# Kernel tuning notes

Measured on AMD Instinct MI355X. Metric: run time of the kernel, lower is better.

## Reference

```python
import jax, jax.numpy as jnp
import numpy as np

H = 1024        # hidden_size
NH = 16         # num_attention_heads
DH = H // NH    # head dim = 64
I = 4096        # intermediate_size
E = 8           # moe_num_experts
B, S = 2, 2048
EPS = 1e-12


def _ln(x, g, b):
    mu = jnp.mean(x, axis=-1, keepdims=True)
    var = jnp.mean(jnp.square(x - mu), axis=-1, keepdims=True)
    return (x - mu) * jax.lax.rsqrt(var + EPS) * g + b


def setup_inputs() -> dict:
    key = jax.random.key(0)
    ks = jax.random.split(key, 16)
    std = 0.02
    p = {
        "hidden_states": jax.random.normal(ks[0], (B, S, H), jnp.float32),
        "Wq": jax.random.normal(ks[1], (H, H), jnp.float32) * std,
        "bq": jnp.zeros((H,), jnp.float32),
        "Wk": jax.random.normal(ks[2], (H, H), jnp.float32) * std,
        "bk": jnp.zeros((H,), jnp.float32),
        "Wv": jax.random.normal(ks[3], (H, H), jnp.float32) * std,
        "bv": jnp.zeros((H,), jnp.float32),
        "Wao": jax.random.normal(ks[4], (H, H), jnp.float32) * std,
        "bao": jnp.zeros((H,), jnp.float32),
        "ln1_g": jnp.ones((H,), jnp.float32),
        "ln1_b": jnp.zeros((H,), jnp.float32),
        "router_w": jax.random.normal(ks[5], (H, E), jnp.float32) * std,
        "We": jax.random.normal(ks[6], (E, H, I), jnp.float32) * std,
        "be": jnp.zeros((E, I), jnp.float32),
        "Wo": jax.random.normal(ks[7], (I, H), jnp.float32) * std,
        "bo": jnp.zeros((H,), jnp.float32),
        "ln2_g": jnp.ones((H,), jnp.float32),
        "ln2_b": jnp.zeros((H,), jnp.float32),
    }
    return p


def reference(hidden_states, Wq, bq, Wk, bk, Wv, bv, Wao, bao, ln1_g, ln1_b,
              router_w, We, be, Wo, bo, ln2_g, ln2_b):
    x = hidden_states  # [B,S,H]

    def heads(t):  # [B,S,H] -> [B,NH,S,DH]
        return t.reshape(B, S, NH, DH).transpose(0, 2, 1, 3)

    q = heads(x @ Wq + bq)
    k = heads(x @ Wk + bk)
    v = heads(x @ Wv + bv)
    scores = jnp.einsum("bhqd,bhkd->bhqk", q, k) / jnp.sqrt(jnp.float32(DH))
    probs = jax.nn.softmax(scores, axis=-1)
    ctx = jnp.einsum("bhqk,bhkd->bhqd", probs, v)
    ctx = ctx.transpose(0, 2, 1, 3).reshape(B, S, H)
    attn_out = _ln(ctx @ Wao + bao + x, ln1_g, ln1_b)  # BertSelfOutput

    # ---- MoE FFN: top-1 routing, per-expert GELU MLP, shared output proj ----
    flat = attn_out.reshape(-1, H)              # [N,H]
    logits = flat @ router_w                    # [N,E]
    idx = jnp.argmax(logits, axis=-1)           # top-1 of softmax == argmax of logits
    inter = jnp.zeros((flat.shape[0], I), flat.dtype)
    for e in range(E):  # small fixed expert count
        h_e = jax.nn.gelu(flat @ We[e] + be[e], approximate=False)
        inter = jnp.where((idx == e)[:, None], h_e, inter)
    inter = inter.reshape(B, S, I)
    out = _ln(inter @ Wo + bo + attn_out, ln2_g, ln2_b)  # BertOutput
    return out
```

## Files before the change

kernel.cpp:

```cpp
#include <hip/hip_runtime.h>
#include <hip/hip_bf16.h>
#include <cstdint>

#define H_  1024
#define NH_ 16
#define DH_ 64
#define I_  4096
#define E_  8
#define B_  2
#define S_  2048
#define N_  4096
#define QKVLD 3072
#define LN_EPS 1e-12f

typedef __attribute__((ext_vector_type(4))) float f4;
typedef __attribute__((ext_vector_type(8))) short s8v;
typedef unsigned int u32;

__device__ __forceinline__ float bf2f(unsigned short u) {
  union { unsigned int i; float f; } c; c.i = ((unsigned int)u) << 16; return c.f;
}
__device__ __forceinline__ unsigned short f2bf(float f) {
  __hip_bfloat16 h = __float2bfloat16(f);
  return *reinterpret_cast<unsigned short*>(&h);
}
__device__ __forceinline__ u32 pack_bf2(float a, float b) {
  return (u32)f2bf(a) | ((u32)f2bf(b) << 16);
}
__device__ __forceinline__ float gelu_f(float x) {
  return 0.5f * x * (1.0f + erff(x * 0.70710678118f));
}
__device__ __forceinline__ void gload16(const void* g, void* l) {
  __builtin_amdgcn_global_load_lds(
      (const __attribute__((address_space(1))) void*)g,
      (__attribute__((address_space(3))) void*)l, 16, 0, 0);
}

__global__ __launch_bounds__(256) void cvt_bf16_kernel(
    const float* __restrict__ in, ushort* __restrict__ out, int n8)
{
  const int t = blockIdx.x * 256 + threadIdx.x;
  if (t >= n8) return;
  const f4 x0 = *(const f4*)(in + (size_t)t * 8);
  const f4 x1 = *(const f4*)(in + (size_t)t * 8 + 4);
  s8v o;
#pragma unroll
  for (int j = 0; j < 4; ++j) { o[j] = (short)f2bf(x0[j]); o[4 + j] = (short)f2bf(x1[j]); }
  *(s8v*)(out + (size_t)t * 8) = o;
}

__global__ __launch_bounds__(256) void transpose_cvt_kernel(
    const float* __restrict__ in, ushort* __restrict__ out, int R, int C)
{
  __shared__ float tile[32][33];
  const size_t zo = (size_t)blockIdx.z * R * C;
  const int bx = blockIdx.x << 5, by = blockIdx.y << 5;
  const int tx = threadIdx.x & 31, ty = threadIdx.x >> 5;
  const float* ip = in + zo + (size_t)by * C + bx;
#pragma unroll
  for (int i = 0; i < 4; ++i)
    tile[ty + 8 * i][tx] = ip[(size_t)(ty + 8 * i) * C + tx];
  __syncthreads();
  ushort* op = out + zo + (size_t)bx * R + by;
#pragma unroll
  for (int i = 0; i < 4; ++i)
    op[(size_t)(ty + 8 * i) * R + tx] = f2bf(tile[tx][ty + 8 * i]);
}

__global__ void concat3_kernel(const float* a, const float* b, const float* c,
                               float* __restrict__ o)
{
  const int t = blockIdx.x * 256 + threadIdx.x;
  if (t < 1024) o[t] = a[t];
  else if (t < 2048) o[t] = b[t - 1024];
  else o[t] = c[t - 2048];
}

__global__ __launch_bounds__(256) void gather_kernel(
    const ushort* __restrict__ X, const int* __restrict__ lists,
    ushort* __restrict__ Xg)
{
  const int r = (blockIdx.x << 1) + (threadIdx.x >> 7);
  const int c = (threadIdx.x & 127) << 3;
  const int tok = lists[r];
  *(s8v*)&Xg[(size_t)r * H_ + c] = *(const s8v*)&X[(size_t)tok * H_ + c];
}

template <bool BF16OUT, int KSPLIT>
__global__ __launch_bounds__(256, 3) void gemm_mfma_kernel(
    const ushort* __restrict__ A, const ushort* __restrict__ Bt,
    const float* __restrict__ bias, void* __restrict__ Cout,
    const int M, const int N, const int K)
{
  __shared__ __align__(16) ushort Asm[2][4][128][8];
  __shared__ __align__(16) ushort Bsm[2][4][128][8];
  const int tid = threadIdx.x;
  const int w = tid >> 6, l = tid & 63;
  const int lq = l & 15, g = l >> 4;
  const int wm = w >> 1, wn = w & 1;
  const int nbx = N >> 7;
  const int nwg = nbx * (M >> 7);
  int id = blockIdx.y * nbx + blockIdx.x;
  id = (id & 7) * (nwg >> 3) + (id >> 3);
  const int m0 = (id / nbx) << 7, n0 = (id % nbx) << 7;
  const int Kspan = K / KSPLIT;
  const int kbase = (KSPLIT > 1) ? blockIdx.z * Kspan : 0;

  const ushort* a0 = A + (size_t)(m0 + l) * K + kbase + (w << 3);
  const ushort* a1 = a0 + (size_t)64 * K;
  const ushort* b0 = Bt + (size_t)(n0 + l) * K + kbase + (w << 3);
  const ushort* b1 = b0 + (size_t)64 * K;

  f4 acc[4][4] = {};
  const int nt = Kspan >> 5;
  gload16(a0, &Asm[0][w][0][0]);  gload16(a1, &Asm[0][w][64][0]);
  gload16(b0, &Bsm[0][w][0][0]);  gload16(b1, &Bsm[0][w][64][0]);
  __syncthreads();
  int cur = 0;
  for (int t = 0; t < nt; ++t) {
    if (t + 1 < nt) {
      const int kt = (t + 1) << 5;
      gload16(a0 + kt, &Asm[cur ^ 1][w][0][0]);
      gload16(a1 + kt, &Asm[cur ^ 1][w][64][0]);
      gload16(b0 + kt, &Bsm[cur ^ 1][w][0][0]);
      gload16(b1 + kt, &Bsm[cur ^ 1][w][64][0]);
    }
    s8v af[4], bfv[4];
#pragma unroll
    for (int mi = 0; mi < 4; ++mi)
      af[mi] = *(const s8v*)&Asm[cur][g][(wm << 6) + (mi << 4) + lq][0];
#pragma unroll
    for (int ni = 0; ni < 4; ++ni)
      bfv[ni] = *(const s8v*)&Bsm[cur][g][(wn << 6) + (ni << 4) + lq][0];
#pragma unroll
    for (int mi = 0; mi < 4; ++mi)
#pragma unroll
      for (int ni = 0; ni < 4; ++ni)
        acc[mi][ni] = __builtin_amdgcn_mfma_f32_16x16x32_bf16(af[mi], bfv[ni], acc[mi][ni], 0, 0, 0);
    __syncthreads();
    cur ^= 1;
  }
  if constexpr (BF16OUT) {
    ushort* st = (ushort*)Asm + (size_t)w * (16 * 72);
    float bs[4];
#pragma unroll
    for (int ni = 0; ni < 4; ++ni) bs[ni] = bias[n0 + (wn << 6) + (ni << 4) + lq];
#pragma unroll
    for (int mi = 0; mi < 4; ++mi) {
#pragma unroll
      for (int ni = 0; ni < 4; ++ni)
#pragma unroll
        for (int r = 0; r < 4; ++r)
          st[((g << 2) + r) * 72 + (ni << 4) + lq] = f2bf(acc[mi][ni][r] + bs[ni]);
#pragma unroll
      for (int q2 = 0; q2 < 2; ++q2) {
        const int r16 = l & 15, ch = (l >> 4) + (q2 << 2);
        const s8v vv = *(const s8v*)&st[r16 * 72 + (ch << 3)];
        *(s8v*)&((ushort*)Cout)[(size_t)(m0 + (wm << 6) + (mi << 4) + r16) * N
                                + n0 + (wn << 6) + (ch << 3)] = vv;
      }
    }
  } else {
    float* outf = (float*)Cout + (size_t)blockIdx.z * M * N;
#pragma unroll
    for (int ni = 0; ni < 4; ++ni) {
      const int col = n0 + (wn << 6) + (ni << 4) + lq;
      const float bs = (KSPLIT == 1 || blockIdx.z == 0) ? bias[col] : 0.f;
#pragma unroll
      for (int mi = 0; mi < 4; ++mi) {
        const int row = m0 + (wm << 6) + (mi << 4) + (g << 2);
#pragma unroll
        for (int r = 0; r < 4; ++r)
          outf[(size_t)(row + r) * N + col] = acc[mi][ni][r] + bs;
      }
    }
  }
}

__global__ __launch_bounds__(256, 3) void moe_mfma_kernel(
    const ushort* __restrict__ Xg, const ushort* __restrict__ WeT,
    const float* __restrict__ be, const int* __restrict__ lists,
    const int* __restrict__ offs, const int* __restrict__ cnt,
    const int* __restrict__ tb, ushort* __restrict__ inter)
{
  __shared__ __align__(16) ushort Asm[2][4][128][8];
  __shared__ __align__(16) ushort Bsm[2][4][128][8];
  __shared__ int tokL[128];
  const int by = blockIdx.y;
  if (by >= tb[E_]) return;
  int e = 0;
#pragma unroll
  for (int t = 1; t < E_; ++t) if (by >= tb[t]) e = t;
  const int rt = by - tb[e];
  const int base = offs[e] + (rt << 7);
  const int nrows = cnt[e] - (rt << 7);
  const int tid = threadIdx.x;
  if (tid < 128) tokL[tid] = (tid < nrows) ? lists[base + tid] : -1;
  __syncthreads();
  const int w = tid >> 6, l = tid & 63;
  const int lq = l & 15, g = l >> 4;
  const int wm = w >> 1, wn = w & 1;
  const int n0 = blockIdx.x << 7;
  const int r0 = min(base + l, N_ - 1);
  const int r1 = min(base + 64 + l, N_ - 1);
  const ushort* a0 = Xg + (size_t)r0 * H_ + (w << 3);
  const ushort* a1 = Xg + (size_t)r1 * H_ + (w << 3);
  const ushort* Wp = WeT + (size_t)e * I_ * H_;
  const ushort* b0 = Wp + (size_t)(n0 + l) * H_ + (w << 3);
  const ushort* b1 = b0 + (size_t)64 * H_;

  f4 acc[4][4] = {};
  gload16(a0, &Asm[0][w][0][0]);  gload16(a1, &Asm[0][w][64][0]);
  gload16(b0, &Bsm[0][w][0][0]);  gload16(b1, &Bsm[0][w][64][0]);
  __syncthreads();
  int cur = 0;
  for (int t = 0; t < 32; ++t) {
    if (t + 1 < 32) {
      const int kt = (t + 1) << 5;
      gload16(a0 + kt, &Asm[cur ^ 1][w][0][0]);
      gload16(a1 + kt, &Asm[cur ^ 1][w][64][0]);
      gload16(b0 + kt, &Bsm[cur ^ 1][w][0][0]);
      gload16(b1 + kt, &Bsm[cur ^ 1][w][64][0]);
    }
    s8v af[4], bfv[4];
#pragma unroll
    for (int mi = 0; mi < 4; ++mi)
      af[mi] = *(const s8v*)&Asm[cur][g][(wm << 6) + (mi << 4) + lq][0];
#pragma unroll
    for (int ni = 0; ni < 4; ++ni)
      bfv[ni] = *(const s8v*)&Bsm[cur][g][(wn << 6) + (ni << 4) + lq][0];
#pragma unroll
    for (int mi = 0; mi < 4; ++mi)
#pragma unroll
      for (int ni = 0; ni < 4; ++ni)
        acc[mi][ni] = __builtin_amdgcn_mfma_f32_16x16x32_bf16(af[mi], bfv[ni], acc[mi][ni], 0, 0, 0);
    __syncthreads();
    cur ^= 1;
  }
  {
    ushort* st = (ushort*)Asm + (size_t)w * (16 * 72);
    float bs[4];
#pragma unroll
    for (int ni = 0; ni < 4; ++ni) bs[ni] = be[(size_t)e * I_ + n0 + (wn << 6) + (ni << 4) + lq];
#pragma unroll
    for (int mi = 0; mi < 4; ++mi) {
#pragma unroll
      for (int ni = 0; ni < 4; ++ni)
#pragma unroll
        for (int r = 0; r < 4; ++r)
          st[((g << 2) + r) * 72 + (ni << 4) + lq] = f2bf(gelu_f(acc[mi][ni][r] + bs[ni]));
#pragma unroll
      for (int q2 = 0; q2 < 2; ++q2) {
        const int r16 = l & 15, ch = (l >> 4) + (q2 << 2);
        const int tok = tokL[(wm << 6) + (mi << 4) + r16];
        if (tok >= 0) {
          const s8v vv = *(const s8v*)&st[r16 * 72 + (ch << 3)];
          *(s8v*)&inter[(size_t)tok * I_ + n0 + (wn << 6) + (ch << 3)] = vv;
        }
      }
    }
  }
}

__global__ __launch_bounds__(256) void attn_mfma_kernel(
    const ushort* __restrict__ qkv, ushort* __restrict__ ctx)
{
  __shared__ __align__(16) ushort Ks[64 * 72];
  __shared__ __align__(16) ushort Vt[64 * 72];
  __shared__ __align__(16) ushort Ps[4][16 * 72];
  const int bid0 = blockIdx.x;
  const int bid  = ((bid0 & 7) << 7) + (bid0 >> 3);
  const int bh = bid >> 5, qt = bid & 31;
  const int b = bh >> 4, h = bh & 15;
  const int tid = threadIdx.x, w = tid >> 6, l = tid & 63;
  const int lq = l & 15, g = l >> 4;
  const size_t bS = (size_t)b * S_;
  const ushort* qb = qkv + bS * QKVLD + h * DH_;
  const ushort* kb = qb + 1024;
  const ushort* vb = qb + 2048;

  s8v qf0, qf1;
  {
    const ushort* qp = qb + (size_t)(qt * 64 + w * 16 + lq) * QKVLD;
    qf0 = *(const s8v*)(qp + (g << 3));
    qf1 = *(const s8v*)(qp + 32 + (g << 3));
  }

  f4 o0 = {0,0,0,0}, o1 = {0,0,0,0}, o2 = {0,0,0,0}, o3 = {0,0,0,0};
  float mrun = -3.0e38f, lrun = 0.f;

  const int skey = tid >> 2;
  const int sd   = (tid & 3) << 4;

  for (int kt = 0; kt < 32; ++kt) {
    __syncthreads();
    {
      const ushort* kp = kb + (size_t)(kt * 64 + skey) * QKVLD + sd;
      *(s8v*)&Ks[skey * 72 + sd]     = *(const s8v*)(kp);
      *(s8v*)&Ks[skey * 72 + sd + 8] = *(const s8v*)(kp + 8);
      const ushort* vp = vb + (size_t)(kt * 64 + skey) * QKVLD + sd;
      const s8v v0 = *(const s8v*)(vp);
      const s8v v1 = *(const s8v*)(vp + 8);
#pragma unroll
      for (int ii = 0; ii < 8; ++ii) {
        Vt[(sd + ii) * 72 + skey]     = v0[ii];
        Vt[(sd + 8 + ii) * 72 + skey] = v1[ii];
      }
    }
    __syncthreads();

    float s[16];
#pragma unroll
    for (int st = 0; st < 4; ++st) {
      f4 acc = {0, 0, 0, 0};
      const s8v ka0 = *(const s8v*)&Ks[(st * 16 + lq) * 72 + (g << 3)];
      const s8v ka1 = *(const s8v*)&Ks[(st * 16 + lq) * 72 + 32 + (g << 3)];
      acc = __builtin_amdgcn_mfma_f32_16x16x32_bf16(ka0, qf0, acc, 0, 0, 0);
      acc = __builtin_amdgcn_mfma_f32_16x16x32_bf16(ka1, qf1, acc, 0, 0, 0);
      s[st * 4 + 0] = acc[0] * 0.125f; s[st * 4 + 1] = acc[1] * 0.125f;
      s[st * 4 + 2] = acc[2] * 0.125f; s[st * 4 + 3] = acc[3] * 0.125f;
    }

    float tmax = s[0];
#pragma unroll
    for (int i = 1; i < 16; ++i) tmax = fmaxf(tmax, s[i]);
    tmax = fmaxf(tmax, __shfl_xor(tmax, 16));
    tmax = fmaxf(tmax, __shfl_xor(tmax, 32));
    const float mnew  = fmaxf(mrun, tmax);
    const float alpha = __expf(mrun - mnew);
    float psum = 0.f;
#pragma unroll
    for (int i = 0; i < 16; ++i) { s[i] = __expf(s[i] - mnew); psum += s[i]; }
    psum += __shfl_xor(psum, 16); psum += __shfl_xor(psum, 32);
    lrun = lrun * alpha + psum; mrun = mnew;

    f4 av;
    av[0] = __shfl(alpha, g * 4 + 0); av[1] = __shfl(alpha, g * 4 + 1);
    av[2] = __shfl(alpha, g * 4 + 2); av[3] = __shfl(alpha, g * 4 + 3);
    o0 *= av; o1 *= av; o2 *= av; o3 *= av;

    {
      ushort* pw = &Ps[w][lq * 72];
#pragma unroll
      for (int st = 0; st < 4; ++st) {
        *(u32*)&pw[st * 16 + g * 4 + 0] = pack_bf2(s[st * 4 + 0], s[st * 4 + 1]);
        *(u32*)&pw[st * 16 + g * 4 + 2] = pack_bf2(s[st * 4 + 2], s[st * 4 + 3]);
      }
    }
    asm volatile("s_waitcnt lgkmcnt(0)" ::: "memory");
    __builtin_amdgcn_sched_barrier(0);

#pragma unroll
    for (int ks = 0; ks < 2; ++ks) {
      const int kof = ks * 32 + (g << 3);
      const s8v pa = *(const s8v*)&Ps[w][lq * 72 + kof];
      const s8v v0 = *(const s8v*)&Vt[( 0 + lq) * 72 + kof];
      const s8v v1 = *(const s8v*)&Vt[(16 + lq) * 72 + kof];
      const s8v v2 = *(const s8v*)&Vt[(32 + lq) * 72 + kof];
      const s8v v3 = *(const s8v*)&Vt[(48 + lq) * 72 + kof];
      o0 = __builtin_amdgcn_mfma_f32_16x16x32_bf16(pa, v0, o0, 0, 0, 0);
      o1 = __builtin_amdgcn_mfma_f32_16x16x32_bf16(pa, v1, o1, 0, 0, 0);
      o2 = __builtin_amdgcn_mfma_f32_16x16x32_bf16(pa, v2, o2, 0, 0, 0);
      o3 = __builtin_amdgcn_mfma_f32_16x16x32_bf16(pa, v3, o3, 0, 0, 0);
    }
  }

  const float inv = 1.f / lrun;
#pragma unroll
  for (int r = 0; r < 4; ++r) {
    const float li = __shfl(inv, g * 4 + r);
    ushort* op = ctx + (bS + (size_t)(qt * 64 + w * 16 + g * 4 + r)) * H_ + h * DH_ + lq;
    op[0]  = f2bf(o0[r] * li);
    op[16] = f2bf(o1[r] * li);
    op[32] = f2bf(o2[r] * li);
    op[48] = f2bf(o3[r] * li);
  }
}

template <int P>
__global__ __launch_bounds__(256) void add_ln_kernel(
    const float* __restrict__ a, const float* __restrict__ r,
    const float* __restrict__ g, const float* __restrict__ bta,
    float* __restrict__ out, ushort* __restrict__ ob)
{
  const int row = blockIdx.x, tid = threadIdx.x;
  const size_t base = (size_t)row * H_;
  const float4 xr = *(const float4*)(r + base + (tid << 2));
  float4 x = xr;
#pragma unroll
  for (int pp = 0; pp < P; ++pp) {
    const float4 xa = *(const float4*)(a + (size_t)pp * N_ * H_ + base + (tid << 2));
    x.x += xa.x; x.y += xa.y; x.z += xa.z; x.w += xa.w;
  }
  float s  = x.x + x.y + x.z + x.w;
  float ss = x.x * x.x + x.y * x.y + x.z * x.z + x.w * x.w;
#pragma unroll
  for (int off = 1; off < 64; off <<= 1) { s += __shfl_xor(s, off); ss += __shfl_xor(ss, off); }
  __shared__ float red[8];
  const int w = tid >> 6, ln = tid & 63;
  if (ln == 0) { red[w] = s; red[4 + w] = ss; }
  __syncthreads();
  const float S  = red[0] + red[1] + red[2] + red[3];
  const float SS = red[4] + red[5] + red[6] + red[7];
  const float mu  = S * (1.f / 1024.f);
  const float var = fmaxf(SS * (1.f / 1024.f) - mu * mu, 0.f);
  const float inv = rsqrtf(var + LN_EPS);
  const float4 gg = *(const float4*)&g[tid << 2];
  const float4 bb = *(const float4*)&bta[tid << 2];
  float4 y;
  y.x = (x.x - mu) * inv * gg.x + bb.x;
  y.y = (x.y - mu) * inv * gg.y + bb.y;
  y.z = (x.z - mu) * inv * gg.z + bb.z;
  y.w = (x.w - mu) * inv * gg.w + bb.w;
  *(float4*)&out[base + (tid << 2)] = y;
  if (ob) {
    ushort4 u;
    u.x = f2bf(y.x); u.y = f2bf(y.y); u.z = f2bf(y.z); u.w = f2bf(y.w);
    *(ushort4*)&ob[base + (tid << 2)] = u;
  }
}

__global__ __launch_bounds__(64) void router_kernel(
    const float* __restrict__ x, const float* __restrict__ rw,
    int* __restrict__ idx, int* __restrict__ cnt)
{
  const int t = blockIdx.x, lane = threadIdx.x;
  float acc[8] = {0.f};
  for (int c = 0; c < H_; c += 64) {
    const float xv = x[(size_t)t * H_ + c + lane];
    const float* wr = rw + (size_t)(c + lane) * E_;
    const float4 w0 = *(const float4*)wr;
    const float4 w1 = *(const float4*)(wr + 4);
    acc[0] += xv * w0.x; acc[1] += xv * w0.y; acc[2] += xv * w0.z; acc[3] += xv * w0.w;
    acc[4] += xv * w1.x; acc[5] += xv * w1.y; acc[6] += xv * w1.z; acc[7] += xv * w1.w;
  }
#pragma unroll
  for (int e = 0; e < E_; ++e) {
    float s = acc[e];
#pragma unroll
    for (int off = 1; off < 64; off <<= 1) s += __shfl_xor(s, off);
    acc[e] = s;
  }
  if (lane == 0) {
    int be_ = 0; float bv = acc[0];
#pragma unroll
    for (int e = 1; e < E_; ++e) if (acc[e] > bv) { bv = acc[e]; be_ = e; }
    idx[t] = be_;
    atomicAdd(&cnt[be_], 1);
  }
}

__global__ void init_kernel(int* cnt) { if (threadIdx.x < E_) cnt[threadIdx.x] = 0; }

__global__ void scan_kernel(const int* __restrict__ cnt, int* __restrict__ offs,
                            int* __restrict__ cursor, int* __restrict__ tb)
{
  int o = 0, tt = 0;
  for (int e = 0; e < E_; ++e) {
    offs[e] = o; cursor[e] = o; tb[e] = tt;
    o += cnt[e]; tt += (cnt[e] + 127) >> 7;
  }
  tb[E_] = tt;
}

__global__ __launch_bounds__(256) void scatter_kernel(
    const int* __restrict__ idx, int* __restrict__ cursor, int* __restrict__ lists)
{
  const int t = blockIdx.x * 256 + threadIdx.x;
  if (t < N_) {
    const int e = idx[t];
    const int p = atomicAdd(&cursor[e], 1);
    lists[p] = t;
  }
}

extern "C" void kernel_launch(void* const* d_in, const int* in_sizes, int n_in,
                              void* d_out, int out_size, void* d_ws, size_t ws_size,
                              hipStream_t stream) {
  const float* x   = (const float*)d_in[0];
  const float* Wq  = (const float*)d_in[1];
  const float* bq  = (const float*)d_in[2];
  const float* Wk  = (const float*)d_in[3];
  const float* bk  = (const float*)d_in[4];
  const float* Wv  = (const float*)d_in[5];
  const float* bv  = (const float*)d_in[6];
  const float* Wao = (const float*)d_in[7];
  const float* bao = (const float*)d_in[8];
  const float* g1  = (const float*)d_in[9];
  const float* b1  = (const float*)d_in[10];
  const float* rw  = (const float*)d_in[11];
  const float* We  = (const float*)d_in[12];
  const float* be  = (const float*)d_in[13];
  const float* Wo  = (const float*)d_in[14];
  const float* bo  = (const float*)d_in[15];
  const float* g2  = (const float*)d_in[16];
  const float* b2  = (const float*)d_in[17];
  float* out = (float*)d_out;

  char* p = (char*)d_ws;
  int* idx    = (int*)p; p += (size_t)N_ * 4;
  int* cnt    = (int*)p; p += 8 * 4;
  int* offs   = (int*)p; p += 8 * 4;
  int* cursor = (int*)p; p += 8 * 4;
  int* tb     = (int*)p; p += 16 * 4;
  int* lists  = (int*)p; p += (size_t)N_ * 4;
  p = (char*)(((uintptr_t)p + 255) & ~(uintptr_t)255);
  const size_t NH = (size_t)N_ * H_;
  ushort* xb     = (ushort*)p; p += NH * 2;
  ushort* qkvb   = (ushort*)p;
  float*  woPart = (float*)p;  p += (size_t)N_ * QKVLD * 2;
  ushort* ctxb   = (ushort*)p; p += NH * 2;
  float*  attn   = (float*)p;  p += NH * 4;
  ushort* attnb  = (ushort*)p; p += NH * 2;
  ushort* interb = (ushort*)p;
  float*  aoPart = (float*)p;  p += (size_t)N_ * I_ * 2;
  ushort* WqkvT  = (ushort*)p; p += (size_t)QKVLD * H_ * 2;
  ushort* WaoT   = (ushort*)p; p += (size_t)H_ * H_ * 2;
  ushort* WoT    = (ushort*)p; p += (size_t)H_ * I_ * 2;
  ushort* WeT    = (ushort*)p; p += (size_t)E_ * I_ * H_ * 2;
  float*  bqkv   = (float*)p;  p += QKVLD * 4;
  ushort* Xg     = xb;

  const dim3 blk(256);

  init_kernel<<<1, 64, 0, stream>>>(cnt);
  cvt_bf16_kernel<<<(N_ * H_ / 8 + 255) / 256, blk, 0, stream>>>(x, xb, N_ * H_ / 8);
  concat3_kernel<<<QKVLD / 256, blk, 0, stream>>>(bq, bk, bv, bqkv);
  transpose_cvt_kernel<<<dim3(32, 32, 1), blk, 0, stream>>>(Wq, WqkvT, H_, H_);
  transpose_cvt_kernel<<<dim3(32, 32, 1), blk, 0, stream>>>(Wk, WqkvT + (size_t)1024 * H_, H_, H_);
  transpose_cvt_kernel<<<dim3(32, 32, 1), blk, 0, stream>>>(Wv, WqkvT + (size_t)2048 * H_, H_, H_);
  transpose_cvt_kernel<<<dim3(32, 32, 1), blk, 0, stream>>>(Wao, WaoT, H_, H_);
  transpose_cvt_kernel<<<dim3(32, 128, 1), blk, 0, stream>>>(Wo, WoT, I_, H_);
  transpose_cvt_kernel<<<dim3(128, 32, 8), blk, 0, stream>>>(We, WeT, H_, I_);

  gemm_mfma_kernel<true, 1><<<dim3(QKVLD / 128, N_ / 128), blk, 0, stream>>>(
      xb, WqkvT, bqkv, qkvb, N_, QKVLD, H_);
  attn_mfma_kernel<<<1024, blk, 0, stream>>>(qkvb, ctxb);
  gemm_mfma_kernel<false, 2><<<dim3(H_ / 128, N_ / 128, 2), blk, 0, stream>>>(
      ctxb, WaoT, bao, aoPart, N_, H_, H_);
  add_ln_kernel<2><<<N_, blk, 0, stream>>>(aoPart, x, g1, b1, attn, attnb);
  router_kernel<<<N_, 64, 0, stream>>>(attn, rw, idx, cnt);
  scan_kernel<<<1, 1, 0, stream>>>(cnt, offs, cursor, tb);
  scatter_kernel<<<N_ / 256, blk, 0, stream>>>(idx, cursor, lists);
  gather_kernel<<<N_ / 2, blk, 0, stream>>>(attnb, lists, Xg);
  moe_mfma_kernel<<<dim3(I_ / 128, N_ / 128 + E_), blk, 0, stream>>>(
      Xg, WeT, be, lists, offs, cnt, tb, interb);
  gemm_mfma_kernel<false, 2><<<dim3(H_ / 128, N_ / 128, 2), blk, 0, stream>>>(
      interb, WoT, bo, woPart, N_, H_, I_);
  add_ln_kernel<2><<<N_, blk, 0, stream>>>(woPart, attn, g2, b2, out, (ushort*)nullptr);
}
```

Baseline: 538.3 us.

## Prefetch two K-tiles ahead with explicit vmcnt waits in GEMM loops

Restructures the double-buffered main loops of the dense GEMM and MoE GEMM kernels so global-to-LDS loads for tile t+2 are issued right after fragments for tile t are read into registers. Explicit s_waitcnt vmcnt and split barriers replace the single __syncthreads, so two tiles of loads are in flight while MFMAs run. Launch bounds are also raised to 4 blocks per CU to encourage higher occupancy. This risks register spills under the tighter bound and depends on the hand-counted vmcnt value matching the number of outstanding loads per stage.

New measurement: 523.4 us. 1.03x faster.

```diff
diff --git a/kernel.cpp b/kernel.cpp
--- a/kernel.cpp
+++ b/kernel.cpp
@@ -87,7 +87,7 @@
 }
 
 template <bool BF16OUT, int KSPLIT>
-__global__ __launch_bounds__(256, 3) void gemm_mfma_kernel(
+__global__ __launch_bounds__(256, 4) void gemm_mfma_kernel(
     const ushort* __restrict__ A, const ushort* __restrict__ Bt,
     const float* __restrict__ bias, void* __restrict__ Cout,
     const int M, const int N, const int K)
@@ -113,18 +113,20 @@
 
   f4 acc[4][4] = {};
   const int nt = Kspan >> 5;
-  gload16(a0, &Asm[0][w][0][0]);  gload16(a1, &Asm[0][w][64][0]);
-  gload16(b0, &Bsm[0][w][0][0]);  gload16(b1, &Bsm[0][w][64][0]);
-  __syncthreads();
-  int cur = 0;
+#define STAGE_G(tt, buf)                                   \
+  { const int kt_ = (tt) << 5;                             \
+    gload16(a0 + kt_, &Asm[buf][w][0][0]);                 \
+    gload16(a1 + kt_, &Asm[buf][w][64][0]);                \
+    gload16(b0 + kt_, &Bsm[buf][w][0][0]);                 \
+    gload16(b1 + kt_, &Bsm[buf][w][64][0]); }
+  STAGE_G(0, 0);
+  STAGE_G(1, 1);
   for (int t = 0; t < nt; ++t) {
-    if (t + 1 < nt) {
-      const int kt = (t + 1) << 5;
-      gload16(a0 + kt, &Asm[cur ^ 1][w][0][0]);
-      gload16(a1 + kt, &Asm[cur ^ 1][w][64][0]);
-      gload16(b0 + kt, &Bsm[cur ^ 1][w][0][0]);
-      gload16(b1 + kt, &Bsm[cur ^ 1][w][64][0]);
-    }
+    const int cur = t & 1;
+    if (t + 1 < nt) { asm volatile("s_waitcnt vmcnt(4)" ::: "memory"); }
+    else            { asm volatile("s_waitcnt vmcnt(0)" ::: "memory"); }
+    __builtin_amdgcn_s_barrier();
+    __builtin_amdgcn_sched_barrier(0);
     s8v af[4], bfv[4];
 #pragma unroll
     for (int mi = 0; mi < 4; ++mi)
@@ -132,14 +134,18 @@
 #pragma unroll
     for (int ni = 0; ni < 4; ++ni)
       bfv[ni] = *(const s8v*)&Bsm[cur][g][(wn << 6) + (ni << 4) + lq][0];
+    asm volatile("s_waitcnt lgkmcnt(0)" ::: "memory");
+    __builtin_amdgcn_sched_barrier(0);
+    __builtin_amdgcn_s_barrier();
+    __builtin_amdgcn_sched_barrier(0);
+    if (t + 2 < nt) STAGE_G(t + 2, cur);
 #pragma unroll
     for (int mi = 0; mi < 4; ++mi)
 #pragma unroll
       for (int ni = 0; ni < 4; ++ni)
         acc[mi][ni] = __builtin_amdgcn_mfma_f32_16x16x32_bf16(af[mi], bfv[ni], acc[mi][ni], 0, 0, 0);
-    __syncthreads();
-    cur ^= 1;
-  }
+  }
+#undef STAGE_G
   if constexpr (BF16OUT) {
     ushort* st = (ushort*)Asm + (size_t)w * (16 * 72);
     float bs[4];
@@ -177,7 +183,7 @@
   }
 }
 
-__global__ __launch_bounds__(256, 3) void moe_mfma_kernel(
+__global__ __launch_bounds__(256, 4) void moe_mfma_kernel(
     const ushort* __restrict__ Xg, const ushort* __restrict__ WeT,
     const float* __restrict__ be, const int* __restrict__ lists,
     const int* __restrict__ offs, const int* __restrict__ cnt,
@@ -210,18 +216,20 @@
   const ushort* b1 = b0 + (size_t)64 * H_;
 
   f4 acc[4][4] = {};
-  gload16(a0, &Asm[0][w][0][0]);  gload16(a1, &Asm[0][w][64][0]);
-  gload16(b0, &Bsm[0][w][0][0]);  gload16(b1, &Bsm[0][w][64][0]);
-  __syncthreads();
-  int cur = 0;
+#define STAGE_M(tt, buf)                                   \
+  { const int kt_ = (tt) << 5;                             \
+    gload16(a0 + kt_, &Asm[buf][w][0][0]);                 \
+    gload16(a1 + kt_, &Asm[buf][w][64][0]);                \
+    gload16(b0 + kt_, &Bsm[buf][w][0][0]);                 \
+    gload16(b1 + kt_, &Bsm[buf][w][64][0]); }
+  STAGE_M(0, 0);
+  STAGE_M(1, 1);
   for (int t = 0; t < 32; ++t) {
-    if (t + 1 < 32) {
-      const int kt = (t + 1) << 5;
-      gload16(a0 + kt, &Asm[cur ^ 1][w][0][0]);
-      gload16(a1 + kt, &Asm[cur ^ 1][w][64][0]);
-      gload16(b0 + kt, &Bsm[cur ^ 1][w][0][0]);
-      gload16(b1 + kt, &Bsm[cur ^ 1][w][64][0]);
-    }
+    const int cur = t & 1;
+    if (t + 1 < 32) { asm volatile("s_waitcnt vmcnt(4)" ::: "memory"); }
+    else            { asm volatile("s_waitcnt vmcnt(0)" ::: "memory"); }
+    __builtin_amdgcn_s_barrier();
+    __builtin_amdgcn_sched_barrier(0);
     s8v af[4], bfv[4];
 #pragma unroll
     for (int mi = 0; mi < 4; ++mi)
@@ -229,14 +237,18 @@
 #pragma unroll
     for (int ni = 0; ni < 4; ++ni)
       bfv[ni] = *(const s8v*)&Bsm[cur][g][(wn << 6) + (ni << 4) + lq][0];
+    asm volatile("s_waitcnt lgkmcnt(0)" ::: "memory");
+    __builtin_amdgcn_sched_barrier(0);
+    __builtin_amdgcn_s_barrier();
+    __builtin_amdgcn_sched_barrier(0);
+    if (t + 2 < 32) STAGE_M(t + 2, cur);
 #pragma unroll
     for (int mi = 0; mi < 4; ++mi)
 #pragma unroll
       for (int ni = 0; ni < 4; ++ni)
         acc[mi][ni] = __builtin_amdgcn_mfma_f32_16x16x32_bf16(af[mi], bfv[ni], acc[mi][ni], 0, 0, 0);
-    __syncthreads();
-    cur ^= 1;
-  }
+  }
+#undef STAGE_M
   {
     ushort* st = (ushort*)Asm + (size_t)w * (16 * 72);
     float bs[4];
```
